# Kernel optimization log

Measured on AMD Instinct MI355X. Metric: run time of the kernel, lower is better.

The kernel has to match this reference:

```python
import jax, jax.numpy as jnp
from jax import lax
import numpy as np

INPUT_DIM = 131
H1, H2, N_CLASSES = 64, 32, 4
B, T = 2048, 256


def _lstm_scan(x, W_ih, W_hh, b_ih, b_hh, return_seq):
    """PyTorch-compatible single-layer LSTM (gate order i,f,g,o), batch_first.
    x: [B,T,D]. Precomputes input projections, scans over time.
    """
    Bx = x.shape[0]
    H = W_hh.shape[1]
    # [B,T,4H] input contribution (both biases folded in, like torch)
    x_proj = jnp.einsum('btd,gd->btg', x, W_ih) + b_ih + b_hh
    W_hh_T = W_hh.T  # [H,4H]

    def step(carry, xt):
        h, c = carry
        gates = xt + h @ W_hh_T  # [B,4H]
        i, f, g, o = jnp.split(gates, 4, axis=-1)
        i = jax.nn.sigmoid(i)
        f = jax.nn.sigmoid(f)
        g = jnp.tanh(g)
        o = jax.nn.sigmoid(o)
        c = f * c + i * g
        h = o * jnp.tanh(c)
        return (h, c), (h if return_seq else None)

    h0 = jnp.zeros((Bx, H), x.dtype)
    (hT, _), hs = lax.scan(step, (h0, h0), jnp.swapaxes(x_proj, 0, 1))
    if return_seq:
        return jnp.swapaxes(hs, 0, 1)  # [B,T,H]
    return hT  # [B,H]


def setup_inputs() -> dict:
    key = jax.random.key(0)
    ks = jax.random.split(key, 12)
    s1 = 1.0 / np.sqrt(H1)
    s2 = 1.0 / np.sqrt(H2)

    def u(k, shape, s):
        return jax.random.uniform(k, shape, jnp.float32, -s, s)

    return {
        'x': jax.random.normal(ks[0], (B, T, INPUT_DIM), jnp.float32),
        'W_ih1': u(ks[1], (4 * H1, INPUT_DIM), s1),
        'W_hh1': u(ks[2], (4 * H1, H1), s1),
        'b_ih1': u(ks[3], (4 * H1,), s1),
        'b_hh1': u(ks[4], (4 * H1,), s1),
        'W_ih2': u(ks[5], (4 * H2, H1), s2),
        'W_hh2': u(ks[6], (4 * H2, H2), s2),
        'b_ih2': u(ks[7], (4 * H2,), s2),
        'b_hh2': u(ks[8], (4 * H2,), s2),
        'W_fc': u(ks[9], (N_CLASSES, H2), s2),
        'b_fc': u(ks[10], (N_CLASSES,), s2),
    }


def reference(x, W_ih1, W_hh1, b_ih1, b_hh1, W_ih2, W_hh2, b_ih2, b_hh2, W_fc, b_fc):
    h1 = _lstm_scan(x, W_ih1, W_hh1, b_ih1, b_hh1, return_seq=True)   # [B,T,64]
    h2_last = _lstm_scan(h1, W_ih2, W_hh2, b_ih2, b_hh2, return_seq=False)  # [B,32]
    return h2_last @ W_fc.T + b_fc  # [B,4]
```

## Files before the change

### kernel.cpp

```cpp
#include <hip/hip_runtime.h>
#include <math.h>

#define B_TOT 2048
#define T_LEN 256
#define D_IN  131
#define NTHR  512

typedef __attribute__((ext_vector_type(8))) short s16x8;
typedef __attribute__((ext_vector_type(4))) float f32x4;

#define MFMA_B16(a,b,c) __builtin_amdgcn_mfma_f32_16x16x32_bf16(a, b, c, 0, 0, 0)

#define PLX   (2*32*168)
#define PLH1  (24*72)
#define PLH2  (24*40)

#define WS_WIH1_LO 40960
#define WS_WHH1    81920
#define WS_W2      114688
#define PREP_N     (40960 + 16384 + 12288)

__device__ __forceinline__ float rcp_(float x){ return __builtin_amdgcn_rcpf(x); }
__device__ __forceinline__ float sigmoidf_(float x){ return rcp_(1.0f + __expf(-x)); }
__device__ __forceinline__ float tanhf_(float x){
    float ax = fabsf(x);
    float e  = __expf(-2.0f * ax);
    float t  = (1.0f - e) * rcp_(1.0f + e);
    return copysignf(t, x);
}
__device__ __forceinline__ unsigned short bfrne(float f){
    unsigned u = __float_as_uint(f);
    return (unsigned short)((u + 0x7fffu + ((u>>16)&1u)) >> 16);
}
__device__ __forceinline__ float bf2f(unsigned short h){
    return __uint_as_float(((unsigned)h)<<16);
}

__global__ void prep_w(const float* __restrict__ W_ih1, const float* __restrict__ W_hh1,
                       const float* __restrict__ W_ih2, const float* __restrict__ W_hh2,
                       const float* __restrict__ b_ih1, const float* __restrict__ b_hh1,
                       short* __restrict__ wsS) {
    int i = blockIdx.x*256 + threadIdx.x;
    if (i >= PREP_N) return;
    if (i < 40960) {
        int np = i / 160, k = i - np*160;
        int u = (np>>5)*8 + (np&7);
        int gate = ((np>>4)&1)*2 + ((np>>3)&1);
        int n = gate*64 + u;
        float v;
        if (k < D_IN)       v = W_ih1[n*D_IN + k];
        else if (k == D_IN) v = b_ih1[n] + b_hh1[n];
        else                v = 0.0f;
        unsigned short hi = bfrne(v);
        wsS[i]              = (short)hi;
        wsS[WS_WIH1_LO + i] = (short)bfrne(v - bf2f(hi));
    } else if (i < 40960 + 16384) {
        int j = i - 40960;
        int np = j >> 6, k = j & 63;
        int u = (np>>5)*8 + (np&7);
        int gate = ((np>>4)&1)*2 + ((np>>3)&1);
        int n = gate*64 + u;
        float v = W_hh1[n*64 + k];
        unsigned short hi = bfrne(v);
        wsS[WS_WHH1 + j]         = (short)hi;
        wsS[WS_WHH1 + 16384 + j] = (short)bfrne(v - bf2f(hi));
    } else {
        int j = i - (40960 + 16384);
        int np = j / 96, k = j - np*96;
        int u = ((np>>5)&3)*8 + (np&7);
        int gate = ((np>>4)&1)*2 + ((np>>3)&1);
        int n = gate*32 + u;
        float v = (k < 64) ? W_ih2[n*64 + k] : W_hh2[n*32 + (k - 64)];
        unsigned short hi = bfrne(v);
        wsS[WS_W2 + j]         = (short)hi;
        wsS[WS_W2 + 12288 + j] = (short)bfrne(v - bf2f(hi));
    }
}

#define PHASE1(U, P) do { \
  const short* h1r = h1bf + (P)*PLH1; \
  short*       h1w = h1bf + (1-(P))*PLH1; \
  const int rH = (r & 7) + 16*(((r >> 3) ^ (P)) & 1); \
  const int rL = 8 + (r & 7) + 8*(((r >> 3) ^ (P)) & 1); \
  s16x8 ah0 = *(const s16x8*)&h1r[rH*72 + g4*8]; \
  s16x8 ah1 = *(const s16x8*)&h1r[rH*72 + 32 + g4*8]; \
  s16x8 al0 = *(const s16x8*)&h1r[rL*72 + g4*8]; \
  s16x8 al1 = *(const s16x8*)&h1r[rL*72 + 32 + g4*8]; \
  accw[U][0] = MFMA_B16(ah0, whf[0][0][0], accw[U][0]); \
  accw[U][1] = MFMA_B16(ah0, whf[1][0][0], accw[U][1]); \
  accw[U][0] = MFMA_B16(ah1, whf[0][1][0], accw[U][0]); \
  accw[U][1] = MFMA_B16(ah1, whf[1][1][0], accw[U][1]); \
  accw[U][0] = MFMA_B16(ah0, whf[0][0][1], accw[U][0]); \
  accw[U][1] = MFMA_B16(ah0, whf[1][0][1], accw[U][1]); \
  accw[U][0] = MFMA_B16(ah1, whf[0][1][1], accw[U][0]); \
  accw[U][1] = MFMA_B16(ah1, whf[1][1][1], accw[U][1]); \
  accw[U][0] = MFMA_B16(al0, whf[0][0][0], accw[U][0]); \
  accw[U][1] = MFMA_B16(al0, whf[1][0][0], accw[U][1]); \
  accw[U][0] = MFMA_B16(al1, whf[0][1][0], accw[U][0]); \
  accw[U][1] = MFMA_B16(al1, whf[1][1][0], accw[U][1]); \
  if ((g4 >> 1) == (P)) { \
    *(f32x4*)(gw0 + 4*(g4 & 1)) = accw[U][0]; \
    *(f32x4*)(gw1 + 4*(g4 & 1)) = accw[U][1]; \
  } \
  float gi = sigmoidf_(gp[0]);      \
  float gf = sigmoidf_(gp[64]); \
  float gg = tanhf_   (gp[128]); \
  float go = sigmoidf_(gp[192]); \
  c1 = gf * c1 + gi * gg; \
  float hv = go * tanhf_(c1); \
  unsigned short hh = bfrne(hv); \
  h1w[bq*72 + u1g]     = (short)hh; \
  h1w[(8+bq)*72 + u1g] = (short)bfrne(hv - bf2f(hh)); \
} while(0)

#define PHASE2(P) do { \
  const short* h1n = h1bf + (1-(P))*PLH1; \
  const short* h2r = h2bf + (P)*PLH2; \
  short*       h2w = h2bf + (1-(P))*PLH2; \
  const int rH2 = (r & 7) + 16*(r >> 3); \
  const int rL2 = 8 + (r & 7) + 8*(r >> 3); \
  s16x8 ah0 = *(const s16x8*)&h1n[rH2*72 + g4*8]; \
  s16x8 ah1 = *(const s16x8*)&h1n[rH2*72 + 32 + g4*8]; \
  s16x8 al0 = *(const s16x8*)&h1n[rL2*72 + g4*8]; \
  s16x8 al1 = *(const s16x8*)&h1n[rL2*72 + 32 + g4*8]; \
  s16x8 bh  = *(const s16x8*)&h2r[rH2*40 + g4*8]; \
  s16x8 bl  = *(const s16x8*)&h2r[rL2*40 + g4*8]; \
  f32x4 p0 = zero4, p1 = zero4; \
  p0 = MFMA_B16(ah0, w2f[0][0][0], p0);  p1 = MFMA_B16(ah0, w2f[1][0][0], p1); \
  p0 = MFMA_B16(ah1, w2f[0][1][0], p0);  p1 = MFMA_B16(ah1, w2f[1][1][0], p1); \
  p0 = MFMA_B16(bh,  w2f[0][2][0], p0);  p1 = MFMA_B16(bh,  w2f[1][2][0], p1); \
  p0 = MFMA_B16(ah0, w2f[0][0][1], p0);  p1 = MFMA_B16(ah0, w2f[1][0][1], p1); \
  p0 = MFMA_B16(ah1, w2f[0][1][1], p0);  p1 = MFMA_B16(ah1, w2f[1][1][1], p1); \
  p0 = MFMA_B16(bh,  w2f[0][2][1], p0);  p1 = MFMA_B16(bh,  w2f[1][2][1], p1); \
  p0 = MFMA_B16(al0, w2f[0][0][0], p0);  p1 = MFMA_B16(al0, w2f[1][0][0], p1); \
  p0 = MFMA_B16(al1, w2f[0][1][0], p0);  p1 = MFMA_B16(al1, w2f[1][1][0], p1); \
  p0 = MFMA_B16(bl,  w2f[0][2][0], p0);  p1 = MFMA_B16(bl,  w2f[1][2][0], p1); \
  if (g4 < 2) { \
    *(f32x4*)(gw0 + 4*g4) = p0; \
    *(f32x4*)(gw1 + 4*g4) = p1; \
  } \
  float gi = sigmoidf_(gp[0]   + l2bi); \
  float gf = sigmoidf_(gp[64]  + l2bf); \
  float gg = tanhf_   (gp[128] + l2bg); \
  float go = sigmoidf_(gp[192] + l2bo); \
  c2 = gf * c2 + gi * gg; \
  float hv = go * tanhf_(c2); \
  h2last = hv; \
  unsigned short hh = bfrne(hv); \
  h2w[bq*40 + u2i]     = (short)hh; \
  h2w[(8+bq)*40 + u2i] = (short)bfrne(hv - bf2f(hh)); \
} while(0)

#define STAGE(S) do { \
  if (w0 < 63) { \
    _Pragma("unroll") \
    for (int m = 0; m < 5; ++m) { \
      if (m < 4 || sv4) { \
        int mrow = (S)*8 + runm[m]; \
        unsigned short hh = bfrne(xr[m]); \
        xn[mrow*168 + km[m]]      = (short)hh; \
        xn[(32+mrow)*168 + km[m]] = (short)bfrne(xr[m] - bf2f(hh)); \
      } \
    } \
    if ((S) < 3 || w0 <= 61) { \
      int tl = ((S) < 3) ? ((w0+1)*4 + (S) + 1) : ((w0+2)*4); \
      _Pragma("unroll") \
      for (int m = 0; m < 5; ++m) \
        if (m < 4 || sv4) xr[m] = x[(size_t)(offm[m] + tl*131)]; \
    } \
  } \
} while(0)

__global__ __launch_bounds__(NTHR, 1) void lstm_mfma(
    const float* __restrict__ x,
    const short* __restrict__ wsS,
    const float* __restrict__ b_ih2, const float* __restrict__ b_hh2,
    const float* __restrict__ W_fc,  const float* __restrict__ b_fc,
    float* __restrict__ out)
{
    __shared__ __attribute__((aligned(16))) short xbf[2*PLX];
    __shared__ __attribute__((aligned(16))) short h1bf[2*PLH1];
    __shared__ __attribute__((aligned(16))) short h2bf[2*PLH2];
    __shared__ __attribute__((aligned(16))) float gpre[2048];

    const int tid  = threadIdx.x;
    const int b0   = blockIdx.x * 8;
    const int w    = tid >> 6;
    const int lane = tid & 63;
    const int r    = lane & 15;
    const int g4   = lane >> 4;
    const int up   = lane & 7;
    const int bq   = lane >> 3;
    const int u1g  = w*8 + up;
    const int u2i  = (w & 3)*8 + up;
    const f32x4 zero4 = {0.f, 0.f, 0.f, 0.f};

    float* gw0 = gpre + ((w*2 + 0)*16 + r)*8;
    float* gw1 = gpre + ((w*2 + 1)*16 + r)*8;
    const float* gp = gpre + (w*32 + up)*8 + bq;

    for (int i = tid; i < 2*PLX/2;  i += NTHR) ((int*)xbf)[i]  = 0;
    for (int i = tid; i < 2*PLH1/2; i += NTHR) ((int*)h1bf)[i] = 0;
    for (int i = tid; i < 2*PLH2/2; i += NTHR) ((int*)h2bf)[i] = 0;
    if (tid < 64) {
        int bf_ = tid >> 5, m = tid & 31;
        xbf[bf_*PLX + m*168 + 131] = (short)0x3f80;
    }

    s16x8 wbf[5][2];
    s16x8 wlo[5][2];
    s16x8 whf[2][2][2];
    s16x8 w2f[2][3][2];
    #pragma unroll
    for (int kt = 0; kt < 5; ++kt)
      #pragma unroll
      for (int nt = 0; nt < 2; ++nt) {
        wbf[kt][nt] = *(const s16x8*)(wsS + (w*32 + nt*16 + r)*160 + kt*32 + g4*8);
        wlo[kt][nt] = *(const s16x8*)(wsS + WS_WIH1_LO + (w*32 + nt*16 + r)*160 + kt*32 + g4*8);
      }
    #pragma unroll
    for (int nt = 0; nt < 2; ++nt)
      #pragma unroll
      for (int kt = 0; kt < 2; ++kt)
        #pragma unroll
        for (int sp = 0; sp < 2; ++sp)
          whf[nt][kt][sp] = *(const s16x8*)(wsS + WS_WHH1 + sp*16384 +
                                            (w*32 + nt*16 + r)*64 + kt*32 + g4*8);
    #pragma unroll
    for (int nt = 0; nt < 2; ++nt)
      #pragma unroll
      for (int kt = 0; kt < 3; ++kt)
        #pragma unroll
        for (int sp = 0; sp < 2; ++sp)
          w2f[nt][kt][sp] = *(const s16x8*)(wsS + WS_W2 + sp*12288 +
                                            ((w&3)*32 + nt*16 + r)*96 + kt*32 + g4*8);

    const float l2bi = b_ih2[u2i]      + b_hh2[u2i];
    const float l2bf = b_ih2[32 + u2i] + b_hh2[32 + u2i];
    const float l2bg = b_ih2[64 + u2i] + b_hh2[64 + u2i];
    const float l2bo = b_ih2[96 + u2i] + b_hh2[96 + u2i];

    float c1 = 0.0f, c2 = 0.0f, h2last = 0.0f;

    const int t2 = tid & 255;
    int runm[5], km[5], offm[5];
    const bool sv4 = (t2 < 24);
    #pragma unroll
    for (int m = 0; m < 5; ++m) {
        int j = t2 + 256*m;
        int rn = j / 131;
        runm[m] = rn; km[m] = j - rn*131;
        offm[m] = (b0 + rn)*33536 + km[m];
    }
    float xr[5] = {0.f,0.f,0.f,0.f,0.f};

    __syncthreads();

    for (int i = tid; i < 4192; i += NTHR) {
        int rn = i / 524; int rem = i - rn*524;
        int tr = rem / 131; int k = rem - tr*131;
        float v = x[(size_t)(b0 + rn)*33536 + tr*131 + k];
        int mrow = tr*8 + rn;
        unsigned short hh = bfrne(v);
        xbf[mrow*168 + k]      = (short)hh;
        xbf[(32+mrow)*168 + k] = (short)bfrne(v - bf2f(hh));
    }
    if (w >= 4) {
        #pragma unroll
        for (int m = 0; m < 5; ++m)
            if (m < 4 || sv4) xr[m] = x[(size_t)(offm[m] + 4*131)];
    }
    __syncthreads();

    f32x4 accw[2][2];

    for (int w0 = 0; w0 < 64; ++w0) {
        const int cur = w0 & 1;
        const short* xc = xbf + cur*PLX;
        short* xn = xbf + (cur^1)*PLX;

        #pragma unroll
        for (int u = 0; u < 2; ++u)
          #pragma unroll
          for (int nt = 0; nt < 2; ++nt) accw[u][nt] = zero4;
        #pragma unroll
        for (int kt = 0; kt < 5; ++kt) {
          #pragma unroll
          for (int u = 0; u < 2; ++u) {
            s16x8 xh = *(const s16x8*)&xc[(u*16 + r)*168 + kt*32 + g4*8];
            s16x8 xl = *(const s16x8*)&xc[(32 + u*16 + r)*168 + kt*32 + g4*8];
            accw[u][0] = MFMA_B16(xh, wbf[kt][0], accw[u][0]);
            accw[u][1] = MFMA_B16(xh, wbf[kt][1], accw[u][1]);
            accw[u][0] = MFMA_B16(xl, wbf[kt][0], accw[u][0]);
            accw[u][1] = MFMA_B16(xl, wbf[kt][1], accw[u][1]);
            accw[u][0] = MFMA_B16(xh, wlo[kt][0], accw[u][0]);
            accw[u][1] = MFMA_B16(xh, wlo[kt][1], accw[u][1]);
          }
        }

        PHASE1(0, 0);
        __syncthreads();
        if (w < 4) { PHASE2(0); } else { STAGE(0); }

        PHASE1(0, 1);
        __syncthreads();
        if (w < 4) { PHASE2(1); } else { STAGE(1); }

        PHASE1(1, 0);
        __syncthreads();
        if (w < 4) { PHASE2(0); } else { STAGE(2); }

        PHASE1(1, 1);
        __syncthreads();
        if (w < 4) { PHASE2(1); } else { STAGE(3); }

        __syncthreads();
    }

    if (w < 4) gpre[bq*32 + u2i] = h2last;
    __syncthreads();
    if (tid < 32) {
        int b = tid >> 2, cls = tid & 3;
        float s = b_fc[cls];
        #pragma unroll
        for (int k2 = 0; k2 < 32; ++k2) s += gpre[b*32 + k2] * W_fc[cls*32 + k2];
        out[(size_t)(b0 + b)*4 + cls] = s;
    }
}

extern "C" void kernel_launch(void* const* d_in, const int* in_sizes, int n_in,
                              void* d_out, int out_size, void* d_ws, size_t ws_size,
                              hipStream_t stream) {
    const float* x     = (const float*)d_in[0];
    const float* W_ih1 = (const float*)d_in[1];
    const float* W_hh1 = (const float*)d_in[2];
    const float* b_ih1 = (const float*)d_in[3];
    const float* b_hh1 = (const float*)d_in[4];
    const float* W_ih2 = (const float*)d_in[5];
    const float* W_hh2 = (const float*)d_in[6];
    const float* b_ih2 = (const float*)d_in[7];
    const float* b_hh2 = (const float*)d_in[8];
    const float* W_fc  = (const float*)d_in[9];
    const float* b_fc  = (const float*)d_in[10];
    float* out = (float*)d_out;
    short* wsS = (short*)d_ws;

    prep_w<<<(PREP_N + 255)/256, 256, 0, stream>>>(W_ih1, W_hh1, W_ih2, W_hh2,
                                                   b_ih1, b_hh1, wsS);
    lstm_mfma<<<B_TOT/8, NTHR, 0, stream>>>(x, wsS, b_ih2, b_hh2, W_fc, b_fc, out);
}
```

Measured before the change: 316.2 us.

## Double block to 1024 threads, halving per-wave gate columns in both LSTM layers

Raises the block from 8 to 16 waves. Each wave now owns one 16-column N tile (4 units × 4 gates) instead of two, and the prep kernel's weight permutation changes to match. Layer-2 work moves to 8 waves, split across two accumulators. Only half of each wave's lanes run the gate nonlinearity, and an extra barrier is added after every phase. The aim is to shorten the serial per-timestep MFMA chain by spreading it over more waves, at the cost of more barriers, idle lanes and a smaller register budget per thread.

Result: slower. 599.9 us (+89.7%).

```diff
diff --git a/kernel.cpp b/kernel.cpp
--- a/kernel.cpp
+++ b/kernel.cpp
@@ -4,7 +4,7 @@
 #define B_TOT 2048
 #define T_LEN 256
 #define D_IN  131
-#define NTHR  512
+#define NTHR  1024
 
 typedef __attribute__((ext_vector_type(8))) short s16x8;
 typedef __attribute__((ext_vector_type(4))) float f32x4;
@@ -44,9 +44,8 @@
     if (i >= PREP_N) return;
     if (i < 40960) {
         int np = i / 160, k = i - np*160;
-        int u = (np>>5)*8 + (np&7);
-        int gate = ((np>>4)&1)*2 + ((np>>3)&1);
-        int n = gate*64 + u;
+        int wv = np >> 4, c = np & 15;
+        int n = (c >> 2)*64 + wv*4 + (c & 3);
         float v;
         if (k < D_IN)       v = W_ih1[n*D_IN + k];
         else if (k == D_IN) v = b_ih1[n] + b_hh1[n];
@@ -57,9 +56,8 @@
     } else if (i < 40960 + 16384) {
         int j = i - 40960;
         int np = j >> 6, k = j & 63;
-        int u = (np>>5)*8 + (np&7);
-        int gate = ((np>>4)&1)*2 + ((np>>3)&1);
-        int n = gate*64 + u;
+        int wv = np >> 4, c = np & 15;
+        int n = (c >> 2)*64 + wv*4 + (c & 3);
         float v = W_hh1[n*64 + k];
         unsigned short hi = bfrne(v);
         wsS[WS_WHH1 + j]         = (short)hi;
@@ -67,9 +65,8 @@
     } else {
         int j = i - (40960 + 16384);
         int np = j / 96, k = j - np*96;
-        int u = ((np>>5)&3)*8 + (np&7);
-        int gate = ((np>>4)&1)*2 + ((np>>3)&1);
-        int n = gate*32 + u;
+        int wv = np >> 4, c = np & 15;
+        int n = (c >> 2)*32 + wv*4 + (c & 3);
         float v = (k < 64) ? W_ih2[n*64 + k] : W_hh2[n*32 + (k - 64)];
         unsigned short hi = bfrne(v);
         wsS[WS_W2 + j]         = (short)hi;
@@ -86,31 +83,25 @@
   s16x8 ah1 = *(const s16x8*)&h1r[rH*72 + 32 + g4*8]; \
   s16x8 al0 = *(const s16x8*)&h1r[rL*72 + g4*8]; \
   s16x8 al1 = *(const s16x8*)&h1r[rL*72 + 32 + g4*8]; \
-  accw[U][0] = MFMA_B16(ah0, whf[0][0][0], accw[U][0]); \
-  accw[U][1] = MFMA_B16(ah0, whf[1][0][0], accw[U][1]); \
-  accw[U][0] = MFMA_B16(ah1, whf[0][1][0], accw[U][0]); \
-  accw[U][1] = MFMA_B16(ah1, whf[1][1][0], accw[U][1]); \
-  accw[U][0] = MFMA_B16(ah0, whf[0][0][1], accw[U][0]); \
-  accw[U][1] = MFMA_B16(ah0, whf[1][0][1], accw[U][1]); \
-  accw[U][0] = MFMA_B16(ah1, whf[0][1][1], accw[U][0]); \
-  accw[U][1] = MFMA_B16(ah1, whf[1][1][1], accw[U][1]); \
-  accw[U][0] = MFMA_B16(al0, whf[0][0][0], accw[U][0]); \
-  accw[U][1] = MFMA_B16(al0, whf[1][0][0], accw[U][1]); \
-  accw[U][0] = MFMA_B16(al1, whf[0][1][0], accw[U][0]); \
-  accw[U][1] = MFMA_B16(al1, whf[1][1][0], accw[U][1]); \
-  if ((g4 >> 1) == (P)) { \
-    *(f32x4*)(gw0 + 4*(g4 & 1)) = accw[U][0]; \
-    *(f32x4*)(gw1 + 4*(g4 & 1)) = accw[U][1]; \
+  accw[U] = MFMA_B16(ah0, whf[0][0], accw[U]); \
+  accw[U] = MFMA_B16(ah1, whf[1][0], accw[U]); \
+  accw[U] = MFMA_B16(ah0, whf[0][1], accw[U]); \
+  accw[U] = MFMA_B16(ah1, whf[1][1], accw[U]); \
+  accw[U] = MFMA_B16(al0, whf[0][0], accw[U]); \
+  accw[U] = MFMA_B16(al1, whf[1][0], accw[U]); \
+  if ((g4 >> 1) == (P)) \
+    *(f32x4*)(gw + 4*(g4 & 1)) = accw[U]; \
+  if (lane < 32) { \
+    float gi = sigmoidf_(gp[0]);     \
+    float gf = sigmoidf_(gp[32]); \
+    float gg = tanhf_   (gp[64]); \
+    float go = sigmoidf_(gp[96]); \
+    c1 = gf * c1 + gi * gg; \
+    float hv = go * tanhf_(c1); \
+    unsigned short hh = bfrne(hv); \
+    h1w[bq*72 + u1]     = (short)hh; \
+    h1w[(8+bq)*72 + u1] = (short)bfrne(hv - bf2f(hh)); \
   } \
-  float gi = sigmoidf_(gp[0]);      \
-  float gf = sigmoidf_(gp[64]); \
-  float gg = tanhf_   (gp[128]); \
-  float go = sigmoidf_(gp[192]); \
-  c1 = gf * c1 + gi * gg; \
-  float hv = go * tanhf_(c1); \
-  unsigned short hh = bfrne(hv); \
-  h1w[bq*72 + u1g]     = (short)hh; \
-  h1w[(8+bq)*72 + u1g] = (short)bfrne(hv - bf2f(hh)); \
 } while(0)
 
 #define PHASE2(P) do { \
@@ -125,53 +116,53 @@
   s16x8 al1 = *(const s16x8*)&h1n[rL2*72 + 32 + g4*8]; \
   s16x8 bh  = *(const s16x8*)&h2r[rH2*40 + g4*8]; \
   s16x8 bl  = *(const s16x8*)&h2r[rL2*40 + g4*8]; \
-  f32x4 p0 = zero4, p1 = zero4; \
-  p0 = MFMA_B16(ah0, w2f[0][0][0], p0);  p1 = MFMA_B16(ah0, w2f[1][0][0], p1); \
-  p0 = MFMA_B16(ah1, w2f[0][1][0], p0);  p1 = MFMA_B16(ah1, w2f[1][1][0], p1); \
-  p0 = MFMA_B16(bh,  w2f[0][2][0], p0);  p1 = MFMA_B16(bh,  w2f[1][2][0], p1); \
-  p0 = MFMA_B16(ah0, w2f[0][0][1], p0);  p1 = MFMA_B16(ah0, w2f[1][0][1], p1); \
-  p0 = MFMA_B16(ah1, w2f[0][1][1], p0);  p1 = MFMA_B16(ah1, w2f[1][1][1], p1); \
-  p0 = MFMA_B16(bh,  w2f[0][2][1], p0);  p1 = MFMA_B16(bh,  w2f[1][2][1], p1); \
-  p0 = MFMA_B16(al0, w2f[0][0][0], p0);  p1 = MFMA_B16(al0, w2f[1][0][0], p1); \
-  p0 = MFMA_B16(al1, w2f[0][1][0], p0);  p1 = MFMA_B16(al1, w2f[1][1][0], p1); \
-  p0 = MFMA_B16(bl,  w2f[0][2][0], p0);  p1 = MFMA_B16(bl,  w2f[1][2][0], p1); \
-  if (g4 < 2) { \
-    *(f32x4*)(gw0 + 4*g4) = p0; \
-    *(f32x4*)(gw1 + 4*g4) = p1; \
+  f32x4 p0 = zero4, q0 = zero4; \
+  p0 = MFMA_B16(ah0, w2f[0][0], p0);  q0 = MFMA_B16(ah0, w2f[0][1], q0); \
+  p0 = MFMA_B16(ah1, w2f[1][0], p0);  q0 = MFMA_B16(ah1, w2f[1][1], q0); \
+  p0 = MFMA_B16(bh,  w2f[2][0], p0);  q0 = MFMA_B16(bh,  w2f[2][1], q0); \
+  p0 = MFMA_B16(al0, w2f[0][0], p0);  q0 = MFMA_B16(al1, w2f[1][0], q0); \
+  p0 = MFMA_B16(bl,  w2f[2][0], p0); \
+  if (g4 < 2) \
+    *(f32x4*)(gw + 4*g4) = p0 + q0; \
+  if (lane < 32) { \
+    float gi = sigmoidf_(gp[0]   + l2bi); \
+    float gf = sigmoidf_(gp[32]  + l2bf); \
+    float gg = tanhf_   (gp[64]  + l2bg); \
+    float go = sigmoidf_(gp[96]  + l2bo); \
+    c2 = gf * c2 + gi * gg; \
+    float hv = go * tanhf_(c2); \
+    h2last = hv; \
+    unsigned short hh = bfrne(hv); \
+    h2w[bq*40 + u2]     = (short)hh; \
+    h2w[(8+bq)*40 + u2] = (short)bfrne(hv - bf2f(hh)); \
   } \
-  float gi = sigmoidf_(gp[0]   + l2bi); \
-  float gf = sigmoidf_(gp[64]  + l2bf); \
-  float gg = tanhf_   (gp[128] + l2bg); \
-  float go = sigmoidf_(gp[192] + l2bo); \
-  c2 = gf * c2 + gi * gg; \
-  float hv = go * tanhf_(c2); \
-  h2last = hv; \
-  unsigned short hh = bfrne(hv); \
-  h2w[bq*40 + u2i]     = (short)hh; \
-  h2w[(8+bq)*40 + u2i] = (short)bfrne(hv - bf2f(hh)); \
 } while(0)
 
 #define STAGE(S) do { \
   if (w0 < 63) { \
     _Pragma("unroll") \
-    for (int m = 0; m < 5; ++m) { \
-      if (m < 4 || sv4) { \
-        int mrow = (S)*8 + runm[m]; \
+    for (int m = 0; m < 3; ++m) { \
+      if (m < 2 || sv24) { \
+        int rn = rk[m] >> 16, kk = rk[m] & 0xffff; \
+        int mrow = (S)*8 + rn; \
         unsigned short hh = bfrne(xr[m]); \
-        xn[mrow*168 + km[m]]      = (short)hh; \
-        xn[(32+mrow)*168 + km[m]] = (short)bfrne(xr[m] - bf2f(hh)); \
+        xn[mrow*168 + kk]      = (short)hh; \
+        xn[(32+mrow)*168 + kk] = (short)bfrne(xr[m] - bf2f(hh)); \
       } \
     } \
     if ((S) < 3 || w0 <= 61) { \
       int tl = ((S) < 3) ? ((w0+1)*4 + (S) + 1) : ((w0+2)*4); \
       _Pragma("unroll") \
-      for (int m = 0; m < 5; ++m) \
-        if (m < 4 || sv4) xr[m] = x[(size_t)(offm[m] + tl*131)]; \
+      for (int m = 0; m < 3; ++m) \
+        if (m < 2 || sv24) { \
+          int rn = rk[m] >> 16, kk = rk[m] & 0xffff; \
+          xr[m] = x[(size_t)((b0 + rn)*33536 + kk + tl*131)]; \
+        } \
     } \
   } \
 } while(0)
 
-__global__ __launch_bounds__(NTHR, 1) void lstm_mfma(
+__global__ __launch_bounds__(NTHR) void lstm_mfma(
     const float* __restrict__ x,
     const short* __restrict__ wsS,
     const float* __restrict__ b_ih2, const float* __restrict__ b_hh2,
@@ -189,72 +180,65 @@
     const int lane = tid & 63;
     const int r    = lane & 15;
     const int g4   = lane >> 4;
-    const int up   = lane & 7;
-    const int bq   = lane >> 3;
-    const int u1g  = w*8 + up;
-    const int u2i  = (w & 3)*8 + up;
+    const int uu   = lane & 3;
+    const int bq   = (lane >> 2) & 7;
+    const int u1   = w*4 + uu;
+    const int u2   = (w & 7)*4 + uu;
     const f32x4 zero4 = {0.f, 0.f, 0.f, 0.f};
 
-    float* gw0 = gpre + ((w*2 + 0)*16 + r)*8;
-    float* gw1 = gpre + ((w*2 + 1)*16 + r)*8;
-    const float* gp = gpre + (w*32 + up)*8 + bq;
+    float* gw = gpre + w*128 + r*8;
+    const float* gp = gpre + w*128 + uu*8 + bq;
 
     for (int i = tid; i < 2*PLX/2;  i += NTHR) ((int*)xbf)[i]  = 0;
     for (int i = tid; i < 2*PLH1/2; i += NTHR) ((int*)h1bf)[i] = 0;
     for (int i = tid; i < 2*PLH2/2; i += NTHR) ((int*)h2bf)[i] = 0;
+
+    s16x8 wbf[5];
+    s16x8 wlo[5];
+    s16x8 whf[2][2];
+    s16x8 w2f[3][2];
+    #pragma unroll
+    for (int kt = 0; kt < 5; ++kt) {
+        wbf[kt] = *(const s16x8*)(wsS + (w*16 + r)*160 + kt*32 + g4*8);
+        wlo[kt] = *(const s16x8*)(wsS + WS_WIH1_LO + (w*16 + r)*160 + kt*32 + g4*8);
+    }
+    #pragma unroll
+    for (int kt = 0; kt < 2; ++kt)
+      #pragma unroll
+      for (int sp = 0; sp < 2; ++sp)
+        whf[kt][sp] = *(const s16x8*)(wsS + WS_WHH1 + sp*16384 +
+                                      (w*16 + r)*64 + kt*32 + g4*8);
+    #pragma unroll
+    for (int kt = 0; kt < 3; ++kt)
+      #pragma unroll
+      for (int sp = 0; sp < 2; ++sp)
+        w2f[kt][sp] = *(const s16x8*)(wsS + WS_W2 + sp*12288 +
+                                      ((w & 7)*16 + r)*96 + kt*32 + g4*8);
+
+    const float l2bi = b_ih2[u2]      + b_hh2[u2];
+    const float l2bf = b_ih2[32 + u2] + b_hh2[32 + u2];
+    const float l2bg = b_ih2[64 + u2] + b_hh2[64 + u2];
+    const float l2bo = b_ih2[96 + u2] + b_hh2[96 + u2];
+
+    float c1 = 0.0f, c2 = 0.0f, h2last = 0.0f;
+
+    const int t2 = tid & 511;
+    const bool sv24 = (t2 < 24);
+    int rk[3];
+    #pragma unroll
+    for (int m = 0; m < 3; ++m) {
+        int j = t2 + 512*m;
+        int rn = j / 131;
+        rk[m] = (rn << 16) | (j - rn*131);
+    }
+    float xr[3] = {0.f, 0.f, 0.f};
+
+    __syncthreads();
+
     if (tid < 64) {
         int bf_ = tid >> 5, m = tid & 31;
         xbf[bf_*PLX + m*168 + 131] = (short)0x3f80;
     }
-
-    s16x8 wbf[5][2];
-    s16x8 wlo[5][2];
-    s16x8 whf[2][2][2];
-    s16x8 w2f[2][3][2];
-    #pragma unroll
-    for (int kt = 0; kt < 5; ++kt)
-      #pragma unroll
-      for (int nt = 0; nt < 2; ++nt) {
-        wbf[kt][nt] = *(const s16x8*)(wsS + (w*32 + nt*16 + r)*160 + kt*32 + g4*8);
-        wlo[kt][nt] = *(const s16x8*)(wsS + WS_WIH1_LO + (w*32 + nt*16 + r)*160 + kt*32 + g4*8);
-      }
-    #pragma unroll
-    for (int nt = 0; nt < 2; ++nt)
-      #pragma unroll
-      for (int kt = 0; kt < 2; ++kt)
-        #pragma unroll
-        for (int sp = 0; sp < 2; ++sp)
-          whf[nt][kt][sp] = *(const s16x8*)(wsS + WS_WHH1 + sp*16384 +
-                                            (w*32 + nt*16 + r)*64 + kt*32 + g4*8);
-    #pragma unroll
-    for (int nt = 0; nt < 2; ++nt)
-      #pragma unroll
-      for (int kt = 0; kt < 3; ++kt)
-        #pragma unroll
-        for (int sp = 0; sp < 2; ++sp)
-          w2f[nt][kt][sp] = *(const s16x8*)(wsS + WS_W2 + sp*12288 +
-                                            ((w&3)*32 + nt*16 + r)*96 + kt*32 + g4*8);
-
-    const float l2bi = b_ih2[u2i]      + b_hh2[u2i];
-    const float l2bf = b_ih2[32 + u2i] + b_hh2[32 + u2i];
-    const float l2bg = b_ih2[64 + u2i] + b_hh2[64 + u2i];
-    const float l2bo = b_ih2[96 + u2i] + b_hh2[96 + u2i];
-
-    float c1 = 0.0f, c2 = 0.0f, h2last = 0.0f;
-
-    const int t2 = tid & 255;
-    int runm[5], km[5], offm[5];
-    const bool sv4 = (t2 < 24);
-    #pragma unroll
-    for (int m = 0; m < 5; ++m) {
-        int j = t2 + 256*m;
-        int rn = j / 131;
-        runm[m] = rn; km[m] = j - rn*131;
-        offm[m] = (b0 + rn)*33536 + km[m];
-    }
-    float xr[5] = {0.f,0.f,0.f,0.f,0.f};
-
-    __syncthreads();
 
     for (int i = tid; i < 4192; i += NTHR) {
         int rn = i / 524; int rem = i - rn*524;
@@ -265,59 +249,58 @@
         xbf[mrow*168 + k]      = (short)hh;
         xbf[(32+mrow)*168 + k] = (short)bfrne(v - bf2f(hh));
     }
-    if (w >= 4) {
+    if (w >= 8) {
         #pragma unroll
-        for (int m = 0; m < 5; ++m)
-            if (m < 4 || sv4) xr[m] = x[(size_t)(offm[m] + 4*131)];
+        for (int m = 0; m < 3; ++m)
+            if (m < 2 || sv24) {
+                int rn = rk[m] >> 16, kk = rk[m] & 0xffff;
+                xr[m] = x[(size_t)((b0 + rn)*33536 + kk + 4*131)];
+            }
     }
     __syncthreads();
 
-    f32x4 accw[2][2];
+    f32x4 accw[2];
 
     for (int w0 = 0; w0 < 64; ++w0) {
         const int cur = w0 & 1;
         const short* xc = xbf + cur*PLX;
         short* xn = xbf + (cur^1)*PLX;
 
-        #pragma unroll
-        for (int u = 0; u < 2; ++u)
-          #pragma unroll
-          for (int nt = 0; nt < 2; ++nt) accw[u][nt] = zero4;
+        accw[0] = zero4; accw[1] = zero4;
         #pragma unroll
         for (int kt = 0; kt < 5; ++kt) {
           #pragma unroll
           for (int u = 0; u < 2; ++u) {
             s16x8 xh = *(const s16x8*)&xc[(u*16 + r)*168 + kt*32 + g4*8];
             s16x8 xl = *(const s16x8*)&xc[(32 + u*16 + r)*168 + kt*32 + g4*8];
-            accw[u][0] = MFMA_B16(xh, wbf[kt][0], accw[u][0]);
-            accw[u][1] = MFMA_B16(xh, wbf[kt][1], accw[u][1]);
-            accw[u][0] = MFMA_B16(xl, wbf[kt][0], accw[u][0]);
-            accw[u][1] = MFMA_B16(xl, wbf[kt][1], accw[u][1]);
-            accw[u][0] = MFMA_B16(xh, wlo[kt][0], accw[u][0]);
-            accw[u][1] = MFMA_B16(xh, wlo[kt][1], accw[u][1]);
+            accw[u] = MFMA_B16(xh, wbf[kt], accw[u]);
+            accw[u] = MFMA_B16(xl, wbf[kt], accw[u]);
+            accw[u] = MFMA_B16(xh, wlo[kt], accw[u]);
           }
         }
 
         PHASE1(0, 0);
         __syncthreads();
-        if (w < 4) { PHASE2(0); } else { STAGE(0); }
+        if (w < 8) { PHASE2(0); } else { STAGE(0); }
+        __syncthreads();
 
         PHASE1(0, 1);
         __syncthreads();
-        if (w < 4) { PHASE2(1); } else { STAGE(1); }
+        if (w < 8) { PHASE2(1); } else { STAGE(1); }
+        __syncthreads();
 
         PHASE1(1, 0);
         __syncthreads();
-        if (w < 4) { PHASE2(0); } else { STAGE(2); }
+        if (w < 8) { PHASE2(0); } else { STAGE(2); }
+        __syncthreads();
 
         PHASE1(1, 1);
         __syncthreads();
-        if (w < 4) { PHASE2(1); } else { STAGE(3); }
-
-        __syncthreads();
-    }
-
-    if (w < 4) gpre[bq*32 + u2i] = h2last;
+        if (w < 8) { PHASE2(1); } else { STAGE(3); }
+        __syncthreads();
+    }
+
+    if (w < 8 && lane < 32) gpre[bq*32 + u2] = h2last;
     __syncthreads();
     if (tid < 32) {
         int b = tid >> 2, cls = tid & 3;
```

## Split LSTM layers onto dedicated warp groups with a one-step skew

Applied to the files above, without the earlier changes.

Raises the block to 12 waves. Eight waves run the layer-1 input projection and recurrence, and four separate waves handle layer 2 plus staging of x. Layer 2 now lags layer 1 by one sub-step, so the two layers overlap instead of alternating within each barrier interval, and one barrier per window is removed. A shared-memory pad is added to force one block per CU. This costs more waves and LDS, and the barrier accounting has to match exactly between the divergent branches.

Result: faster. 303.3 us (-4.1%).

```diff
diff --git a/kernel.cpp b/kernel.cpp
--- a/kernel.cpp
+++ b/kernel.cpp
@@ -4,7 +4,7 @@
 #define B_TOT 2048
 #define T_LEN 256
 #define D_IN  131
-#define NTHR  512
+#define NTHR  768
 
 typedef __attribute__((ext_vector_type(8))) short s16x8;
 typedef __attribute__((ext_vector_type(4))) float f32x4;
@@ -181,7 +181,8 @@
     __shared__ __attribute__((aligned(16))) short xbf[2*PLX];
     __shared__ __attribute__((aligned(16))) short h1bf[2*PLH1];
     __shared__ __attribute__((aligned(16))) short h2bf[2*PLH2];
-    __shared__ __attribute__((aligned(16))) float gpre[2048];
+    __shared__ __attribute__((aligned(16))) float gpre[3072];
+    __shared__ float occ_pad[4672];
 
     const int tid  = threadIdx.x;
     const int b0   = blockIdx.x * 8;
@@ -195,6 +196,8 @@
     const int u2i  = (w & 3)*8 + up;
     const f32x4 zero4 = {0.f, 0.f, 0.f, 0.f};
 
+    if (tid == 0) *(volatile float*)occ_pad = 0.f;
+
     float* gw0 = gpre + ((w*2 + 0)*16 + r)*8;
     float* gw1 = gpre + ((w*2 + 1)*16 + r)*8;
     const float* gp = gpre + (w*32 + up)*8 + bq;
@@ -202,60 +205,15 @@
     for (int i = tid; i < 2*PLX/2;  i += NTHR) ((int*)xbf)[i]  = 0;
     for (int i = tid; i < 2*PLH1/2; i += NTHR) ((int*)h1bf)[i] = 0;
     for (int i = tid; i < 2*PLH2/2; i += NTHR) ((int*)h2bf)[i] = 0;
+
+    float c1 = 0.0f, c2 = 0.0f, h2last = 0.0f;
+
+    __syncthreads();
+
     if (tid < 64) {
         int bf_ = tid >> 5, m = tid & 31;
         xbf[bf_*PLX + m*168 + 131] = (short)0x3f80;
     }
-
-    s16x8 wbf[5][2];
-    s16x8 wlo[5][2];
-    s16x8 whf[2][2][2];
-    s16x8 w2f[2][3][2];
-    #pragma unroll
-    for (int kt = 0; kt < 5; ++kt)
-      #pragma unroll
-      for (int nt = 0; nt < 2; ++nt) {
-        wbf[kt][nt] = *(const s16x8*)(wsS + (w*32 + nt*16 + r)*160 + kt*32 + g4*8);
-        wlo[kt][nt] = *(const s16x8*)(wsS + WS_WIH1_LO + (w*32 + nt*16 + r)*160 + kt*32 + g4*8);
-      }
-    #pragma unroll
-    for (int nt = 0; nt < 2; ++nt)
-      #pragma unroll
-      for (int kt = 0; kt < 2; ++kt)
-        #pragma unroll
-        for (int sp = 0; sp < 2; ++sp)
-          whf[nt][kt][sp] = *(const s16x8*)(wsS + WS_WHH1 + sp*16384 +
-                                            (w*32 + nt*16 + r)*64 + kt*32 + g4*8);
-    #pragma unroll
-    for (int nt = 0; nt < 2; ++nt)
-      #pragma unroll
-      for (int kt = 0; kt < 3; ++kt)
-        #pragma unroll
-        for (int sp = 0; sp < 2; ++sp)
-          w2f[nt][kt][sp] = *(const s16x8*)(wsS + WS_W2 + sp*12288 +
-                                            ((w&3)*32 + nt*16 + r)*96 + kt*32 + g4*8);
-
-    const float l2bi = b_ih2[u2i]      + b_hh2[u2i];
-    const float l2bf = b_ih2[32 + u2i] + b_hh2[32 + u2i];
-    const float l2bg = b_ih2[64 + u2i] + b_hh2[64 + u2i];
-    const float l2bo = b_ih2[96 + u2i] + b_hh2[96 + u2i];
-
-    float c1 = 0.0f, c2 = 0.0f, h2last = 0.0f;
-
-    const int t2 = tid & 255;
-    int runm[5], km[5], offm[5];
-    const bool sv4 = (t2 < 24);
-    #pragma unroll
-    for (int m = 0; m < 5; ++m) {
-        int j = t2 + 256*m;
-        int rn = j / 131;
-        runm[m] = rn; km[m] = j - rn*131;
-        offm[m] = (b0 + rn)*33536 + km[m];
-    }
-    float xr[5] = {0.f,0.f,0.f,0.f,0.f};
-
-    __syncthreads();
-
     for (int i = tid; i < 4192; i += NTHR) {
         int rn = i / 524; int rem = i - rn*524;
         int tr = rem / 131; int k = rem - tr*131;
@@ -265,59 +223,97 @@
         xbf[mrow*168 + k]      = (short)hh;
         xbf[(32+mrow)*168 + k] = (short)bfrne(v - bf2f(hh));
     }
-    if (w >= 4) {
+    __syncthreads();
+
+    if (w < 8) {
+        s16x8 wbf[5][2];
+        s16x8 wlo[5][2];
+        s16x8 whf[2][2][2];
+        #pragma unroll
+        for (int kt = 0; kt < 5; ++kt)
+          #pragma unroll
+          for (int nt = 0; nt < 2; ++nt) {
+            wbf[kt][nt] = *(const s16x8*)(wsS + (w*32 + nt*16 + r)*160 + kt*32 + g4*8);
+            wlo[kt][nt] = *(const s16x8*)(wsS + WS_WIH1_LO + (w*32 + nt*16 + r)*160 + kt*32 + g4*8);
+          }
+        #pragma unroll
+        for (int nt = 0; nt < 2; ++nt)
+          #pragma unroll
+          for (int kt = 0; kt < 2; ++kt)
+            #pragma unroll
+            for (int sp = 0; sp < 2; ++sp)
+              whf[nt][kt][sp] = *(const s16x8*)(wsS + WS_WHH1 + sp*16384 +
+                                                (w*32 + nt*16 + r)*64 + kt*32 + g4*8);
+        f32x4 accw[2][2];
+
+        for (int w0 = 0; w0 < 64; ++w0) {
+            const short* xc = xbf + (w0 & 1)*PLX;
+            #pragma unroll
+            for (int u = 0; u < 2; ++u)
+              #pragma unroll
+              for (int nt = 0; nt < 2; ++nt) accw[u][nt] = zero4;
+            #pragma unroll
+            for (int kt = 0; kt < 5; ++kt) {
+              #pragma unroll
+              for (int u = 0; u < 2; ++u) {
+                s16x8 xh = *(const s16x8*)&xc[(u*16 + r)*168 + kt*32 + g4*8];
+                s16x8 xl = *(const s16x8*)&xc[(32 + u*16 + r)*168 + kt*32 + g4*8];
+                accw[u][0] = MFMA_B16(xh, wbf[kt][0], accw[u][0]);
+                accw[u][1] = MFMA_B16(xh, wbf[kt][1], accw[u][1]);
+                accw[u][0] = MFMA_B16(xl, wbf[kt][0], accw[u][0]);
+                accw[u][1] = MFMA_B16(xl, wbf[kt][1], accw[u][1]);
+                accw[u][0] = MFMA_B16(xh, wlo[kt][0], accw[u][0]);
+                accw[u][1] = MFMA_B16(xh, wlo[kt][1], accw[u][1]);
+              }
+            }
+            PHASE1(0, 0);  __syncthreads();
+            PHASE1(0, 1);  __syncthreads();
+            PHASE1(1, 0);  __syncthreads();
+            PHASE1(1, 1);  __syncthreads();
+        }
+        __syncthreads();
+    } else {
+        s16x8 w2f[2][3][2];
+        #pragma unroll
+        for (int nt = 0; nt < 2; ++nt)
+          #pragma unroll
+          for (int kt = 0; kt < 3; ++kt)
+            #pragma unroll
+            for (int sp = 0; sp < 2; ++sp)
+              w2f[nt][kt][sp] = *(const s16x8*)(wsS + WS_W2 + sp*12288 +
+                                                ((w & 3)*32 + nt*16 + r)*96 + kt*32 + g4*8);
+        const float l2bi = b_ih2[u2i]      + b_hh2[u2i];
+        const float l2bf = b_ih2[32 + u2i] + b_hh2[32 + u2i];
+        const float l2bg = b_ih2[64 + u2i] + b_hh2[64 + u2i];
+        const float l2bo = b_ih2[96 + u2i] + b_hh2[96 + u2i];
+
+        const int t2 = tid & 255;
+        const bool sv4 = (t2 < 24);
+        int runm[5], km[5], offm[5];
+        #pragma unroll
+        for (int m = 0; m < 5; ++m) {
+            int j = t2 + 256*m;
+            int rn = j / 131;
+            runm[m] = rn; km[m] = j - rn*131;
+            offm[m] = (b0 + rn)*33536 + km[m];
+        }
+        float xr[5];
         #pragma unroll
         for (int m = 0; m < 5; ++m)
-            if (m < 4 || sv4) xr[m] = x[(size_t)(offm[m] + 4*131)];
-    }
-    __syncthreads();
-
-    f32x4 accw[2][2];
-
-    for (int w0 = 0; w0 < 64; ++w0) {
-        const int cur = w0 & 1;
-        const short* xc = xbf + cur*PLX;
-        short* xn = xbf + (cur^1)*PLX;
-
-        #pragma unroll
-        for (int u = 0; u < 2; ++u)
-          #pragma unroll
-          for (int nt = 0; nt < 2; ++nt) accw[u][nt] = zero4;
-        #pragma unroll
-        for (int kt = 0; kt < 5; ++kt) {
-          #pragma unroll
-          for (int u = 0; u < 2; ++u) {
-            s16x8 xh = *(const s16x8*)&xc[(u*16 + r)*168 + kt*32 + g4*8];
-            s16x8 xl = *(const s16x8*)&xc[(32 + u*16 + r)*168 + kt*32 + g4*8];
-            accw[u][0] = MFMA_B16(xh, wbf[kt][0], accw[u][0]);
-            accw[u][1] = MFMA_B16(xh, wbf[kt][1], accw[u][1]);
-            accw[u][0] = MFMA_B16(xl, wbf[kt][0], accw[u][0]);
-            accw[u][1] = MFMA_B16(xl, wbf[kt][1], accw[u][1]);
-            accw[u][0] = MFMA_B16(xh, wlo[kt][0], accw[u][0]);
-            accw[u][1] = MFMA_B16(xh, wlo[kt][1], accw[u][1]);
-          }
+            xr[m] = (m < 4 || sv4) ? x[(size_t)(offm[m] + 4*131)] : 0.f;
+
+        for (int w0 = 0; w0 < 64; ++w0) {
+            short* xn = xbf + ((w0 & 1) ^ 1)*PLX;
+            STAGE(0);  if (w0 > 0) PHASE2(1);  __syncthreads();
+            STAGE(1);  PHASE2(0);              __syncthreads();
+            STAGE(2);  PHASE2(1);              __syncthreads();
+            STAGE(3);  PHASE2(0);              __syncthreads();
         }
-
-        PHASE1(0, 0);
+        PHASE2(1);
         __syncthreads();
-        if (w < 4) { PHASE2(0); } else { STAGE(0); }
-
-        PHASE1(0, 1);
-        __syncthreads();
-        if (w < 4) { PHASE2(1); } else { STAGE(1); }
-
-        PHASE1(1, 0);
-        __syncthreads();
-        if (w < 4) { PHASE2(0); } else { STAGE(2); }
-
-        PHASE1(1, 1);
-        __syncthreads();
-        if (w < 4) { PHASE2(1); } else { STAGE(3); }
-
-        __syncthreads();
-    }
-
-    if (w < 4) gpre[bq*32 + u2i] = h2last;
+    }
+
+    if (w >= 8) gpre[bq*32 + u2i] = h2last;
     __syncthreads();
     if (tid < 32) {
         int b = tid >> 2, cls = tid & 3;
```
